# Kernel optimization log

Hardware: AMD Instinct MI355X
Metric: run time of the kernel (lower is better)

## Reference

```python
import jax, jax.numpy as jnp
import numpy as np

HIDDEN = 256
HEADS = 8
HEAD_DIM = HIDDEN // HEADS
BATCH = 2
N_NODES = 8192
N_EDGES = 262144


def setup_inputs() -> dict:
    key = jax.random.key(0)
    ks = jax.random.split(key, 12)
    node_states = jax.random.normal(ks[0], (BATCH, N_NODES, HIDDEN), dtype=jnp.float32)
    b_idx = jax.random.randint(ks[1], (N_EDGES,), 0, BATCH)
    s_idx = jax.random.randint(ks[2], (N_EDGES,), 0, N_NODES)
    t_idx = jax.random.randint(ks[3], (N_EDGES,), 0, N_NODES)
    edge_indices = jnp.stack([b_idx, s_idx, t_idx]).astype(jnp.int64)
    edge_values = jax.random.normal(ks[4], (N_EDGES, HIDDEN), dtype=jnp.float32)
    scale = 1.0 / np.sqrt(HIDDEN)
    Wq = jax.random.normal(ks[5], (HIDDEN, HIDDEN), dtype=jnp.float32) * scale
    bq = jnp.zeros((HIDDEN,), jnp.float32)
    Wk = jax.random.normal(ks[6], (HIDDEN, HIDDEN), dtype=jnp.float32) * scale
    bk = jnp.zeros((HIDDEN,), jnp.float32)
    Wv = jax.random.normal(ks[7], (HIDDEN, HIDDEN), dtype=jnp.float32) * scale
    bv = jnp.zeros((HIDDEN,), jnp.float32)
    We = jax.random.normal(ks[8], (HIDDEN, HIDDEN), dtype=jnp.float32) * scale
    be = jnp.zeros((HIDDEN,), jnp.float32)
    return {"node_states": node_states, "edge_indices": edge_indices, "edge_values": edge_values,
            "Wq": Wq, "bq": bq, "Wk": Wk, "bk": bk, "Wv": Wv, "bv": bv, "We": We, "be": be}


def reference(node_states, edge_indices, edge_values, Wq, bq, Wk, bk, Wv, bv, We, be):
    batch, n_nodes, hidden = node_states.shape
    E = edge_indices.shape[1]
    b_idx, s_idx, t_idx = edge_indices[0], edge_indices[1], edge_indices[2]

    # Dense QKV projections over nodes (torch Linear: x @ W.T + b)
    Q = node_states @ Wq.T + bq
    K = node_states @ Wk.T + bk
    V = node_states @ Wv.T + bv

    # Gather per-edge query/key/value, split heads -> (E, H, D)
    Qm = Q[b_idx, s_idx].reshape(E, HEADS, HEAD_DIM)
    Kn = K[b_idx, t_idx].reshape(E, HEADS, HEAD_DIM)
    Vn = V[b_idx, t_idx].reshape(E, HEADS, HEAD_DIM)

    # Edge feature projections (use_edge_values=True path)
    Ke = (edge_values @ Wk.T + bk).reshape(E, HEADS, HEAD_DIM)
    Ve = (edge_values @ We.T + be).reshape(E, HEADS, HEAD_DIM)

    inv_sqrt_d = 1.0 / jnp.sqrt(jnp.float32(HEAD_DIM))
    # node2node + node2edge = Qm.(Kn+Ke)/sqrt(d)  -> (E, H)
    logits = jnp.sum(Qm * (Kn + Ke), axis=-1) * inv_sqrt_d

    # torch.sparse.softmax(..., dim=-1): dim -1 of (B,N,N,H) is the DENSE heads
    # dim, so softmax is taken over the heads axis of the per-edge values.
    attn = jax.nn.softmax(logits, axis=-1)  # (E, H)

    out_edges = (attn[..., None] * (Vn + Ve)).reshape(E, hidden)  # (E, hidden)

    # Scatter-sum edges to their (batch, src) node: sparse.mm with 0/1 mask
    seg = b_idx * n_nodes + s_idx
    flat = jax.ops.segment_sum(out_edges, seg, num_segments=batch * n_nodes)
    return flat.reshape(batch, n_nodes, hidden)
```

## Files before the change

### kernel.cpp

```cpp
#include <hip/hip_runtime.h>
#include <hip/hip_bf16.h>

#define HID 256
#define NN 8192
#define NE 262144

typedef float f32x4 __attribute__((ext_vector_type(4)));
typedef __bf16 bf16x8 __attribute__((ext_vector_type(8)));
typedef __bf16 bf16x4 __attribute__((ext_vector_type(4)));

__global__ void conv_weights(const float* __restrict__ wq, const float* __restrict__ wk,
                             const float* __restrict__ wv, const float* __restrict__ we,
                             __bf16* __restrict__ o) {
    int i = blockIdx.x * 256 + threadIdx.x;
    const float* srcs[4] = {wq, wk, wv, we};
    int m = i >> 16;
    int j = i & 65535;
    o[i] = (__bf16)srcs[m][j];
}

__device__ __forceinline__ void stage_tile(const float* __restrict__ src, char* lb, int tid) {
    const float4* xs = (const float4*)src;
    #pragma unroll
    for (int kq = 0; kq < 16; ++kq) {
        int f = tid + kq * 256;
        int row = f >> 6, c4 = f & 63;
        float4 v = xs[f];
        bf16x4 h;
        h[0] = (__bf16)v.x; h[1] = (__bf16)v.y; h[2] = (__bf16)v.z; h[3] = (__bf16)v.w;
        int off = (row * 512 + c4 * 8) ^ ((row & 7) << 4);
        *(bf16x4*)(lb + off) = h;
    }
}

__global__ void qkv_gemm(const float* __restrict__ x,
                         const __bf16* __restrict__ wbf,
                         const float* __restrict__ bq, const float* __restrict__ bk,
                         const float* __restrict__ bv,
                         __bf16* __restrict__ qbf, __bf16* __restrict__ kbf,
                         __bf16* __restrict__ vbf) {
    __shared__ __bf16 xt[64 * 256];
    char* lb = (char*)xt;
    int tid = threadIdx.x;
    int blk = blockIdx.x;

    stage_tile(x + (size_t)blk * 64 * 256, lb, tid);
    __syncthreads();

    int w = tid >> 6, lane = tid & 63;
    int l15 = lane & 15, l4 = lane >> 4;
    int cw = w * 64;
    const float* biases[3] = {bq, bk, bv};
    __bf16* outs[3] = {qbf, kbf, vbf};

    for (int m = 0; m < 3; ++m) {
        const __bf16* W = wbf + (size_t)m * 65536;
        f32x4 acc[4][4] = {};
        for (int ks = 0; ks < 8; ++ks) {
            bf16x8 aW[4], bE[4];
            #pragma unroll
            for (int tn = 0; tn < 4; ++tn)
                aW[tn] = *(const bf16x8*)(W + (size_t)(cw + tn * 16 + l15) * 256 + ks * 32 + l4 * 8);
            #pragma unroll
            for (int te = 0; te < 4; ++te) {
                int row = te * 16 + l15;
                int off = (row * 512 + ks * 64 + l4 * 16) ^ ((row & 7) << 4);
                bE[te] = *(const bf16x8*)(lb + off);
            }
            #pragma unroll
            for (int tn = 0; tn < 4; ++tn)
                #pragma unroll
                for (int te = 0; te < 4; ++te)
                    acc[tn][te] = __builtin_amdgcn_mfma_f32_16x16x32_bf16(aW[tn], bE[te], acc[tn][te], 0, 0, 0);
        }
        __bf16* out = outs[m];
        #pragma unroll
        for (int tn = 0; tn < 4; ++tn) {
            float4 b4 = *(const float4*)(biases[m] + cw + tn * 16 + l4 * 4);
            #pragma unroll
            for (int te = 0; te < 4; ++te) {
                int row = blk * 64 + te * 16 + l15;
                int col = cw + tn * 16 + l4 * 4;
                bf16x4 h;
                h[0] = (__bf16)(acc[tn][te][0] + b4.x);
                h[1] = (__bf16)(acc[tn][te][1] + b4.y);
                h[2] = (__bf16)(acc[tn][te][2] + b4.z);
                h[3] = (__bf16)(acc[tn][te][3] + b4.w);
                *(bf16x4*)(out + (size_t)row * 256 + col) = h;
            }
        }
    }
}

__global__ void k_hist(const int* __restrict__ eidx, unsigned* __restrict__ hist) {
    int e = blockIdx.x * 256 + threadIdx.x;
    int key = eidx[e] * NN + eidx[NE + e];
    atomicAdd(&hist[key], 1u);
}

__global__ void k_scan(const unsigned* __restrict__ hist, unsigned* __restrict__ cursor) {
    __shared__ unsigned tot[256];
    int tid = threadIdx.x;
    unsigned s = 0;
    for (int i = 0; i < 64; ++i) s += hist[tid * 64 + i];
    tot[tid] = s;
    __syncthreads();
    for (int d = 1; d < 256; d <<= 1) {
        unsigned v = (tid >= d) ? tot[tid - d] : 0u;
        __syncthreads();
        tot[tid] += v;
        __syncthreads();
    }
    unsigned run = (tid == 0) ? 0u : tot[tid - 1];
    for (int i = 0; i < 64; ++i) {
        int idx = tid * 64 + i;
        cursor[idx] = run;
        run += hist[idx];
    }
}

__global__ void k_perm(const int* __restrict__ eidx, unsigned* __restrict__ cursor,
                       int* __restrict__ perm) {
    int e = blockIdx.x * 256 + threadIdx.x;
    int key = eidx[e] * NN + eidx[NE + e];
    unsigned pos = atomicAdd(&cursor[key], 1u);
    perm[pos] = e;
}

__global__ void edge_logits(const float* __restrict__ ev,
                            const int* __restrict__ eidx,
                            const __bf16* __restrict__ wbf,
                            const float* __restrict__ bkb,
                            const __bf16* __restrict__ qbf, const __bf16* __restrict__ kbf,
                            float* __restrict__ attn_ws) {
    __shared__ __bf16 evt[64 * 256];
    __shared__ int sb[64], ss[64], st[64];
    char* lb = (char*)evt;
    int tid = threadIdx.x;
    int e0 = blockIdx.x * 64;

    stage_tile(ev + (size_t)e0 * 256, lb, tid);
    if (tid < 64) {
        sb[tid] = eidx[e0 + tid];
        ss[tid] = eidx[NE + e0 + tid];
        st[tid] = eidx[2 * NE + e0 + tid];
    }
    __syncthreads();

    int w = tid >> 6, lane = tid & 63;
    int l15 = lane & 15, l4 = lane >> 4;
    int cw = w * 64;

    const __bf16* WK = wbf + 65536;
    f32x4 acc[4][4] = {};
    for (int ks = 0; ks < 8; ++ks) {
        bf16x8 aW[4], bE[4];
        #pragma unroll
        for (int tn = 0; tn < 4; ++tn)
            aW[tn] = *(const bf16x8*)(WK + (size_t)(cw + tn * 16 + l15) * 256 + ks * 32 + l4 * 8);
        #pragma unroll
        for (int te = 0; te < 4; ++te) {
            int row = te * 16 + l15;
            int off = (row * 512 + ks * 64 + l4 * 16) ^ ((row & 7) << 4);
            bE[te] = *(const bf16x8*)(lb + off);
        }
        #pragma unroll
        for (int tn = 0; tn < 4; ++tn)
            #pragma unroll
            for (int te = 0; te < 4; ++te)
                acc[tn][te] = __builtin_amdgcn_mfma_f32_16x16x32_bf16(aW[tn], bE[te], acc[tn][te], 0, 0, 0);
    }
    __syncthreads();

    #pragma unroll
    for (int tn = 0; tn < 4; ++tn) {
        float4 b4 = *(const float4*)(bkb + cw + tn * 16 + l4 * 4);
        #pragma unroll
        for (int te = 0; te < 4; ++te) {
            int edge = te * 16 + l15;
            int colb = (cw + tn * 16 + l4 * 4) * 2;
            bf16x4 h;
            h[0] = (__bf16)(acc[tn][te][0] + b4.x);
            h[1] = (__bf16)(acc[tn][te][1] + b4.y);
            h[2] = (__bf16)(acc[tn][te][2] + b4.z);
            h[3] = (__bf16)(acc[tn][te][3] + b4.w);
            int off = (edge * 512 + colb) ^ ((edge & 7) << 4);
            *(bf16x4*)(lb + off) = h;
        }
    }
    __syncthreads();

    int cl = lane & 31, eh = lane >> 5;
    #pragma unroll
    for (int it = 0; it < 8; ++it) {
        int e = w * 16 + it * 2 + eh;
        int b_ = sb[e], s_ = ss[e], t_ = st[e];
        bf16x8 qv = *(const bf16x8*)(qbf + ((size_t)b_ * NN + s_) * 256 + cl * 8);
        bf16x8 kv = *(const bf16x8*)(kbf + ((size_t)b_ * NN + t_) * 256 + cl * 8);
        int off = (e * 512 + cl * 16) ^ ((e & 7) << 4);
        bf16x8 kev = *(const bf16x8*)(lb + off);
        float val = 0.f;
        #pragma unroll
        for (int j = 0; j < 8; ++j)
            val += (float)qv[j] * ((float)kv[j] + (float)kev[j]);
        val += __shfl_xor(val, 1);
        val += __shfl_xor(val, 2);
        val *= 0.17677669529663687f;
        float mx = val;
        mx = fmaxf(mx, __shfl_xor(mx, 4));
        mx = fmaxf(mx, __shfl_xor(mx, 8));
        mx = fmaxf(mx, __shfl_xor(mx, 16));
        float ex = __expf(val - mx);
        float s4 = ex;
        s4 += __shfl_xor(s4, 4);
        s4 += __shfl_xor(s4, 8);
        s4 += __shfl_xor(s4, 16);
        float a = ex / s4;
        if ((cl & 3) == 0)
            attn_ws[(size_t)(e0 + e) * 8 + (cl >> 2)] = a;
    }
}

__global__ void edge_scatter2(const float* __restrict__ ev,
                              const int* __restrict__ eidx,
                              const __bf16* __restrict__ wbf,
                              const float* __restrict__ beb,
                              const __bf16* __restrict__ vbf,
                              const float* __restrict__ attn_ws,
                              const int* __restrict__ perm,
                              float* __restrict__ out) {
    __shared__ __bf16 evt[64 * 256];
    __shared__ int pe[64], sb[64], ss[64], st[64];
    char* lb = (char*)evt;
    int tid = threadIdx.x;
    int p0 = blockIdx.x * 64;

    if (tid < 64) {
        int e = perm[p0 + tid];
        pe[tid] = e;
        sb[tid] = eidx[e];
        ss[tid] = eidx[NE + e];
        st[tid] = eidx[2 * NE + e];
    }
    __syncthreads();

    #pragma unroll
    for (int kq = 0; kq < 16; ++kq) {
        int f = tid + kq * 256;
        int row = f >> 6, c4 = f & 63;
        const float4* src = (const float4*)(ev + (size_t)pe[row] * 256);
        float4 v = src[c4];
        bf16x4 h;
        h[0] = (__bf16)v.x; h[1] = (__bf16)v.y; h[2] = (__bf16)v.z; h[3] = (__bf16)v.w;
        int off = (row * 512 + c4 * 8) ^ ((row & 7) << 4);
        *(bf16x4*)(lb + off) = h;
    }
    __syncthreads();

    int w = tid >> 6, lane = tid & 63;
    int l15 = lane & 15, l4 = lane >> 4;
    int cw = w * 64;

    const __bf16* WE = wbf + 3 * 65536;
    f32x4 acc[4][4] = {};
    for (int ks = 0; ks < 8; ++ks) {
        bf16x8 aW[4], bE[4];
        #pragma unroll
        for (int tn = 0; tn < 4; ++tn)
            aW[tn] = *(const bf16x8*)(WE + (size_t)(cw + tn * 16 + l15) * 256 + ks * 32 + l4 * 8);
        #pragma unroll
        for (int te = 0; te < 4; ++te) {
            int row = te * 16 + l15;
            int off = (row * 512 + ks * 64 + l4 * 16) ^ ((row & 7) << 4);
            bE[te] = *(const bf16x8*)(lb + off);
        }
        #pragma unroll
        for (int tn = 0; tn < 4; ++tn)
            #pragma unroll
            for (int te = 0; te < 4; ++te)
                acc[tn][te] = __builtin_amdgcn_mfma_f32_16x16x32_bf16(aW[tn], bE[te], acc[tn][te], 0, 0, 0);
    }
    __syncthreads();

    #pragma unroll
    for (int tn = 0; tn < 4; ++tn) {
        float4 b4 = *(const float4*)(beb + cw + tn * 16 + l4 * 4);
        #pragma unroll
        for (int te = 0; te < 4; ++te) {
            int edge = te * 16 + l15;
            int colb = (cw + tn * 16 + l4 * 4) * 2;
            bf16x4 h;
            h[0] = (__bf16)(acc[tn][te][0] + b4.x);
            h[1] = (__bf16)(acc[tn][te][1] + b4.y);
            h[2] = (__bf16)(acc[tn][te][2] + b4.z);
            h[3] = (__bf16)(acc[tn][te][3] + b4.w);
            int off = (edge * 512 + colb) ^ ((edge & 7) << 4);
            *(bf16x4*)(lb + off) = h;
        }
    }
    __syncthreads();

    float a0 = 0.f, a1 = 0.f, a2 = 0.f, a3 = 0.f;
    int havekey = -1;
    size_t obase = 0;
    #pragma unroll
    for (int it = 0; it < 16; ++it) {
        int e = w * 16 + it;
        int ge = pe[e];
        int b_ = sb[e], s_ = ss[e], t_ = st[e];
        const __bf16* vrow = vbf + ((size_t)b_ * NN + t_) * 256;
        int swz = (e & 7) << 4;
        float c0, c1, c2, c3;
        {
            float att, vv, vev;
            int col, off;
            col = lane;             att = attn_ws[(size_t)ge * 8 + 0 + (lane >> 5)];
            vv = (float)vrow[col];  off = (e * 512 + col * 2) ^ swz;
            vev = (float)*(const __bf16*)(lb + off); c0 = att * (vv + vev);
            col = 64 + lane;        att = attn_ws[(size_t)ge * 8 + 2 + (lane >> 5)];
            vv = (float)vrow[col];  off = (e * 512 + col * 2) ^ swz;
            vev = (float)*(const __bf16*)(lb + off); c1 = att * (vv + vev);
            col = 128 + lane;       att = attn_ws[(size_t)ge * 8 + 4 + (lane >> 5)];
            vv = (float)vrow[col];  off = (e * 512 + col * 2) ^ swz;
            vev = (float)*(const __bf16*)(lb + off); c2 = att * (vv + vev);
            col = 192 + lane;       att = attn_ws[(size_t)ge * 8 + 6 + (lane >> 5)];
            vv = (float)vrow[col];  off = (e * 512 + col * 2) ^ swz;
            vev = (float)*(const __bf16*)(lb + off); c3 = att * (vv + vev);
        }
        int key = __builtin_amdgcn_readfirstlane(b_ * NN + s_);
        if (key != havekey) {
            if (havekey >= 0) {
                float* orow = out + obase;
                unsafeAtomicAdd(orow + lane, a0);
                unsafeAtomicAdd(orow + 64 + lane, a1);
                unsafeAtomicAdd(orow + 128 + lane, a2);
                unsafeAtomicAdd(orow + 192 + lane, a3);
            }
            a0 = c0; a1 = c1; a2 = c2; a3 = c3;
            havekey = key;
            obase = (size_t)key * 256;
        } else {
            a0 += c0; a1 += c1; a2 += c2; a3 += c3;
        }
    }
    if (havekey >= 0) {
        float* orow = out + obase;
        unsafeAtomicAdd(orow + lane, a0);
        unsafeAtomicAdd(orow + 64 + lane, a1);
        unsafeAtomicAdd(orow + 128 + lane, a2);
        unsafeAtomicAdd(orow + 192 + lane, a3);
    }
}

extern "C" void kernel_launch(void* const* d_in, const int* in_sizes, int n_in,
                              void* d_out, int out_size, void* d_ws, size_t ws_size,
                              hipStream_t stream) {
    const float* node_states = (const float*)d_in[0];
    const int*   eidx        = (const int*)d_in[1];
    const float* ev          = (const float*)d_in[2];
    const float* Wq          = (const float*)d_in[3];
    const float* bq          = (const float*)d_in[4];
    const float* Wk          = (const float*)d_in[5];
    const float* bk          = (const float*)d_in[6];
    const float* Wv          = (const float*)d_in[7];
    const float* bv          = (const float*)d_in[8];
    const float* We          = (const float*)d_in[9];
    const float* be          = (const float*)d_in[10];
    float* out = (float*)d_out;

    char* ws = (char*)d_ws;
    __bf16*   qbf     = (__bf16*)ws;
    __bf16*   kbf     = (__bf16*)(ws + 8388608);
    __bf16*   vbf     = (__bf16*)(ws + 16777216);
    float*    attn_ws = (float*)(ws + 25165824);
    __bf16*   wbf     = (__bf16*)(ws + 33554432);
    unsigned* hist    = (unsigned*)(ws + 34078720);
    unsigned* cursor  = (unsigned*)(ws + 34144256);
    int*      perm    = (int*)(ws + 34209792);

    hipMemsetAsync(d_out, 0, (size_t)out_size * sizeof(float), stream);
    hipMemsetAsync(hist, 0, 16384 * sizeof(unsigned), stream);
    conv_weights<<<1024, 256, 0, stream>>>(Wq, Wk, Wv, We, wbf);
    qkv_gemm<<<256, 256, 0, stream>>>(node_states, wbf, bq, bk, bv, qbf, kbf, vbf);
    k_hist<<<1024, 256, 0, stream>>>(eidx, hist);
    k_scan<<<1, 256, 0, stream>>>(hist, cursor);
    k_perm<<<1024, 256, 0, stream>>>(eidx, cursor, perm);
    edge_logits<<<4096, 256, 0, stream>>>(ev, eidx, wbf, bk, qbf, kbf, attn_ws);
    edge_scatter2<<<4096, 256, 0, stream>>>(ev, eidx, wbf, be, vbf, attn_ws, perm, out);
}
```

Baseline: 332.9 us.

## Fuse edge logits and scatter kernels, keep attention weights in LDS

Merges the logits and scatter kernels into one kernel that stages each permuted edge tile once, computes the Ke projection and logits straight from MFMA accumulators, and runs the per-edge softmax in shared memory. This removes the second full read and conversion of edge_values and the global attention workspace round-trip. In exchange the kernel holds more live state, which risks register pressure under the occupancy-4 launch bound, and the logits stage now gathers Q/K rows in permuted order.

```diff
diff --git a/kernel.cpp b/kernel.cpp
--- a/kernel.cpp
+++ b/kernel.cpp
@@ -127,110 +127,18 @@
     perm[pos] = e;
 }
 
-__global__ void edge_logits(const float* __restrict__ ev,
-                            const int* __restrict__ eidx,
-                            const __bf16* __restrict__ wbf,
-                            const float* __restrict__ bkb,
-                            const __bf16* __restrict__ qbf, const __bf16* __restrict__ kbf,
-                            float* __restrict__ attn_ws) {
-    __shared__ __bf16 evt[64 * 256];
-    __shared__ int sb[64], ss[64], st[64];
-    char* lb = (char*)evt;
-    int tid = threadIdx.x;
-    int e0 = blockIdx.x * 64;
-
-    stage_tile(ev + (size_t)e0 * 256, lb, tid);
-    if (tid < 64) {
-        sb[tid] = eidx[e0 + tid];
-        ss[tid] = eidx[NE + e0 + tid];
-        st[tid] = eidx[2 * NE + e0 + tid];
-    }
-    __syncthreads();
-
-    int w = tid >> 6, lane = tid & 63;
-    int l15 = lane & 15, l4 = lane >> 4;
-    int cw = w * 64;
-
-    const __bf16* WK = wbf + 65536;
-    f32x4 acc[4][4] = {};
-    for (int ks = 0; ks < 8; ++ks) {
-        bf16x8 aW[4], bE[4];
-        #pragma unroll
-        for (int tn = 0; tn < 4; ++tn)
-            aW[tn] = *(const bf16x8*)(WK + (size_t)(cw + tn * 16 + l15) * 256 + ks * 32 + l4 * 8);
-        #pragma unroll
-        for (int te = 0; te < 4; ++te) {
-            int row = te * 16 + l15;
-            int off = (row * 512 + ks * 64 + l4 * 16) ^ ((row & 7) << 4);
-            bE[te] = *(const bf16x8*)(lb + off);
-        }
-        #pragma unroll
-        for (int tn = 0; tn < 4; ++tn)
-            #pragma unroll
-            for (int te = 0; te < 4; ++te)
-                acc[tn][te] = __builtin_amdgcn_mfma_f32_16x16x32_bf16(aW[tn], bE[te], acc[tn][te], 0, 0, 0);
-    }
-    __syncthreads();
-
-    #pragma unroll
-    for (int tn = 0; tn < 4; ++tn) {
-        float4 b4 = *(const float4*)(bkb + cw + tn * 16 + l4 * 4);
-        #pragma unroll
-        for (int te = 0; te < 4; ++te) {
-            int edge = te * 16 + l15;
-            int colb = (cw + tn * 16 + l4 * 4) * 2;
-            bf16x4 h;
-            h[0] = (__bf16)(acc[tn][te][0] + b4.x);
-            h[1] = (__bf16)(acc[tn][te][1] + b4.y);
-            h[2] = (__bf16)(acc[tn][te][2] + b4.z);
-            h[3] = (__bf16)(acc[tn][te][3] + b4.w);
-            int off = (edge * 512 + colb) ^ ((edge & 7) << 4);
-            *(bf16x4*)(lb + off) = h;
-        }
-    }
-    __syncthreads();
-
-    int cl = lane & 31, eh = lane >> 5;
-    #pragma unroll
-    for (int it = 0; it < 8; ++it) {
-        int e = w * 16 + it * 2 + eh;
-        int b_ = sb[e], s_ = ss[e], t_ = st[e];
-        bf16x8 qv = *(const bf16x8*)(qbf + ((size_t)b_ * NN + s_) * 256 + cl * 8);
-        bf16x8 kv = *(const bf16x8*)(kbf + ((size_t)b_ * NN + t_) * 256 + cl * 8);
-        int off = (e * 512 + cl * 16) ^ ((e & 7) << 4);
-        bf16x8 kev = *(const bf16x8*)(lb + off);
-        float val = 0.f;
-        #pragma unroll
-        for (int j = 0; j < 8; ++j)
-            val += (float)qv[j] * ((float)kv[j] + (float)kev[j]);
-        val += __shfl_xor(val, 1);
-        val += __shfl_xor(val, 2);
-        val *= 0.17677669529663687f;
-        float mx = val;
-        mx = fmaxf(mx, __shfl_xor(mx, 4));
-        mx = fmaxf(mx, __shfl_xor(mx, 8));
-        mx = fmaxf(mx, __shfl_xor(mx, 16));
-        float ex = __expf(val - mx);
-        float s4 = ex;
-        s4 += __shfl_xor(s4, 4);
-        s4 += __shfl_xor(s4, 8);
-        s4 += __shfl_xor(s4, 16);
-        float a = ex / s4;
-        if ((cl & 3) == 0)
-            attn_ws[(size_t)(e0 + e) * 8 + (cl >> 2)] = a;
-    }
-}
-
-__global__ void edge_scatter2(const float* __restrict__ ev,
-                              const int* __restrict__ eidx,
-                              const __bf16* __restrict__ wbf,
-                              const float* __restrict__ beb,
-                              const __bf16* __restrict__ vbf,
-                              const float* __restrict__ attn_ws,
-                              const int* __restrict__ perm,
-                              float* __restrict__ out) {
+__global__ __launch_bounds__(256, 4)
+void edge_fused(const float* __restrict__ ev,
+                const int* __restrict__ eidx,
+                const __bf16* __restrict__ wbf,
+                const float* __restrict__ bkb, const float* __restrict__ beb,
+                const __bf16* __restrict__ qbf, const __bf16* __restrict__ kbf,
+                const __bf16* __restrict__ vbf,
+                const int* __restrict__ perm,
+                float* __restrict__ out) {
     __shared__ __bf16 evt[64 * 256];
     __shared__ int pe[64], sb[64], ss[64], st[64];
+    __shared__ float smx[64 * 8];
     char* lb = (char*)evt;
     int tid = threadIdx.x;
     int p0 = blockIdx.x * 64;
@@ -261,41 +169,113 @@
     int l15 = lane & 15, l4 = lane >> 4;
     int cw = w * 64;
 
-    const __bf16* WE = wbf + 3 * 65536;
-    f32x4 acc[4][4] = {};
-    for (int ks = 0; ks < 8; ++ks) {
-        bf16x8 aW[4], bE[4];
+    {
+        const __bf16* WK = wbf + 65536;
+        f32x4 acc[4][4] = {};
+        for (int ks = 0; ks < 8; ++ks) {
+            bf16x8 aW[4], bE[4];
+            #pragma unroll
+            for (int tn = 0; tn < 4; ++tn)
+                aW[tn] = *(const bf16x8*)(WK + (size_t)(cw + tn * 16 + l15) * 256 + ks * 32 + l4 * 8);
+            #pragma unroll
+            for (int te = 0; te < 4; ++te) {
+                int row = te * 16 + l15;
+                int off = (row * 512 + ks * 64 + l4 * 16) ^ ((row & 7) << 4);
+                bE[te] = *(const bf16x8*)(lb + off);
+            }
+            #pragma unroll
+            for (int tn = 0; tn < 4; ++tn)
+                #pragma unroll
+                for (int te = 0; te < 4; ++te)
+                    acc[tn][te] = __builtin_amdgcn_mfma_f32_16x16x32_bf16(aW[tn], bE[te], acc[tn][te], 0, 0, 0);
+        }
+
+        f32x4 bk4[4];
         #pragma unroll
         for (int tn = 0; tn < 4; ++tn)
-            aW[tn] = *(const bf16x8*)(WE + (size_t)(cw + tn * 16 + l15) * 256 + ks * 32 + l4 * 8);
+            bk4[tn] = *(const f32x4*)(bkb + cw + tn * 16 + l4 * 4);
+
         #pragma unroll
         for (int te = 0; te < 4; ++te) {
-            int row = te * 16 + l15;
-            int off = (row * 512 + ks * 64 + l4 * 16) ^ ((row & 7) << 4);
-            bE[te] = *(const bf16x8*)(lb + off);
-        }
-        #pragma unroll
-        for (int tn = 0; tn < 4; ++tn)
-            #pragma unroll
-            for (int te = 0; te < 4; ++te)
-                acc[tn][te] = __builtin_amdgcn_mfma_f32_16x16x32_bf16(aW[tn], bE[te], acc[tn][te], 0, 0, 0);
-    }
-    __syncthreads();
-
-    #pragma unroll
-    for (int tn = 0; tn < 4; ++tn) {
-        float4 b4 = *(const float4*)(beb + cw + tn * 16 + l4 * 4);
-        #pragma unroll
-        for (int te = 0; te < 4; ++te) {
-            int edge = te * 16 + l15;
-            int colb = (cw + tn * 16 + l4 * 4) * 2;
-            bf16x4 h;
-            h[0] = (__bf16)(acc[tn][te][0] + b4.x);
-            h[1] = (__bf16)(acc[tn][te][1] + b4.y);
-            h[2] = (__bf16)(acc[tn][te][2] + b4.z);
-            h[3] = (__bf16)(acc[tn][te][3] + b4.w);
-            int off = (edge * 512 + colb) ^ ((edge & 7) << 4);
-            *(bf16x4*)(lb + off) = h;
+            int el = te * 16 + l15;
+            int b_ = sb[el], s_ = ss[el], t_ = st[el];
+            const __bf16* qp = qbf + ((size_t)b_ * NN + s_) * 256 + cw + l4 * 4;
+            const __bf16* kp = kbf + ((size_t)b_ * NN + t_) * 256 + cw + l4 * 4;
+            bf16x4 qv[4], kv[4];
+            #pragma unroll
+            for (int tn = 0; tn < 4; ++tn) {
+                qv[tn] = *(const bf16x4*)(qp + tn * 16);
+                kv[tn] = *(const bf16x4*)(kp + tn * 16);
+            }
+            #pragma unroll
+            for (int h = 0; h < 2; ++h) {
+                float val = 0.f;
+                #pragma unroll
+                for (int j = 0; j < 2; ++j) {
+                    int tn = h * 2 + j;
+                    #pragma unroll
+                    for (int r = 0; r < 4; ++r) {
+                        float ke = acc[tn][te][r] + bk4[tn][r];
+                        val += (float)qv[tn][r] * ((float)kv[tn][r] + ke);
+                    }
+                }
+                val += __shfl_xor(val, 16);
+                val += __shfl_xor(val, 32);
+                if (l4 == 0) smx[el * 8 + w * 2 + h] = val * 0.17677669529663687f;
+            }
+        }
+    }
+    __syncthreads();
+
+    if (tid < 64) {
+        float l[8], mx = -1e30f;
+        #pragma unroll
+        for (int h = 0; h < 8; ++h) { l[h] = smx[tid * 8 + h]; mx = fmaxf(mx, l[h]); }
+        float sum = 0.f;
+        #pragma unroll
+        for (int h = 0; h < 8; ++h) { l[h] = __expf(l[h] - mx); sum += l[h]; }
+        float inv = 1.f / sum;
+        #pragma unroll
+        for (int h = 0; h < 8; ++h) smx[tid * 8 + h] = l[h] * inv;
+    }
+
+    {
+        const __bf16* WE = wbf + 3 * 65536;
+        f32x4 acc[4][4] = {};
+        for (int ks = 0; ks < 8; ++ks) {
+            bf16x8 aW[4], bE[4];
+            #pragma unroll
+            for (int tn = 0; tn < 4; ++tn)
+                aW[tn] = *(const bf16x8*)(WE + (size_t)(cw + tn * 16 + l15) * 256 + ks * 32 + l4 * 8);
+            #pragma unroll
+            for (int te = 0; te < 4; ++te) {
+                int row = te * 16 + l15;
+                int off = (row * 512 + ks * 64 + l4 * 16) ^ ((row & 7) << 4);
+                bE[te] = *(const bf16x8*)(lb + off);
+            }
+            #pragma unroll
+            for (int tn = 0; tn < 4; ++tn)
+                #pragma unroll
+                for (int te = 0; te < 4; ++te)
+                    acc[tn][te] = __builtin_amdgcn_mfma_f32_16x16x32_bf16(aW[tn], bE[te], acc[tn][te], 0, 0, 0);
+        }
+        __syncthreads();
+
+        #pragma unroll
+        for (int tn = 0; tn < 4; ++tn) {
+            float4 b4 = *(const float4*)(beb + cw + tn * 16 + l4 * 4);
+            #pragma unroll
+            for (int te = 0; te < 4; ++te) {
+                int edge = te * 16 + l15;
+                int colb = (cw + tn * 16 + l4 * 4) * 2;
+                bf16x4 h;
+                h[0] = (__bf16)(acc[tn][te][0] + b4.x);
+                h[1] = (__bf16)(acc[tn][te][1] + b4.y);
+                h[2] = (__bf16)(acc[tn][te][2] + b4.z);
+                h[3] = (__bf16)(acc[tn][te][3] + b4.w);
+                int off = (edge * 512 + colb) ^ ((edge & 7) << 4);
+                *(bf16x4*)(lb + off) = h;
+            }
         }
     }
     __syncthreads();
@@ -306,7 +286,6 @@
     #pragma unroll
     for (int it = 0; it < 16; ++it) {
         int e = w * 16 + it;
-        int ge = pe[e];
         int b_ = sb[e], s_ = ss[e], t_ = st[e];
         const __bf16* vrow = vbf + ((size_t)b_ * NN + t_) * 256;
         int swz = (e & 7) << 4;
@@ -314,16 +293,16 @@
         {
             float att, vv, vev;
             int col, off;
-            col = lane;             att = attn_ws[(size_t)ge * 8 + 0 + (lane >> 5)];
+            col = lane;             att = smx[e * 8 + 0 + (lane >> 5)];
             vv = (float)vrow[col];  off = (e * 512 + col * 2) ^ swz;
             vev = (float)*(const __bf16*)(lb + off); c0 = att * (vv + vev);
-            col = 64 + lane;        att = attn_ws[(size_t)ge * 8 + 2 + (lane >> 5)];
+            col = 64 + lane;        att = smx[e * 8 + 2 + (lane >> 5)];
             vv = (float)vrow[col];  off = (e * 512 + col * 2) ^ swz;
             vev = (float)*(const __bf16*)(lb + off); c1 = att * (vv + vev);
-            col = 128 + lane;       att = attn_ws[(size_t)ge * 8 + 4 + (lane >> 5)];
+            col = 128 + lane;       att = smx[e * 8 + 4 + (lane >> 5)];
             vv = (float)vrow[col];  off = (e * 512 + col * 2) ^ swz;
             vev = (float)*(const __bf16*)(lb + off); c2 = att * (vv + vev);
-            col = 192 + lane;       att = attn_ws[(size_t)ge * 8 + 6 + (lane >> 5)];
+            col = 192 + lane;       att = smx[e * 8 + 6 + (lane >> 5)];
             vv = (float)vrow[col];  off = (e * 512 + col * 2) ^ swz;
             vev = (float)*(const __bf16*)(lb + off); c3 = att * (vv + vev);
         }
@@ -369,14 +348,13 @@
     float* out = (float*)d_out;
 
     char* ws = (char*)d_ws;
-    __bf16*   qbf     = (__bf16*)ws;
-    __bf16*   kbf     = (__bf16*)(ws + 8388608);
-    __bf16*   vbf     = (__bf16*)(ws + 16777216);
-    float*    attn_ws = (float*)(ws + 25165824);
-    __bf16*   wbf     = (__bf16*)(ws + 33554432);
-    unsigned* hist    = (unsigned*)(ws + 34078720);
-    unsigned* cursor  = (unsigned*)(ws + 34144256);
-    int*      perm    = (int*)(ws + 34209792);
+    __bf16*   qbf    = (__bf16*)ws;
+    __bf16*   kbf    = (__bf16*)(ws + 8388608);
+    __bf16*   vbf    = (__bf16*)(ws + 16777216);
+    __bf16*   wbf    = (__bf16*)(ws + 25165824);
+    unsigned* hist   = (unsigned*)(ws + 25690112);
+    unsigned* cursor = (unsigned*)(ws + 25755648);
+    int*      perm   = (int*)(ws + 25821184);
 
     hipMemsetAsync(d_out, 0, (size_t)out_size * sizeof(float), stream);
     hipMemsetAsync(hist, 0, 16384 * sizeof(unsigned), stream);
@@ -385,6 +363,5 @@
     k_hist<<<1024, 256, 0, stream>>>(eidx, hist);
     k_scan<<<1, 256, 0, stream>>>(hist, cursor);
     k_perm<<<1024, 256, 0, stream>>>(eidx, cursor, perm);
-    edge_logits<<<4096, 256, 0, stream>>>(ev, eidx, wbf, bk, qbf, kbf, attn_ws);
-    edge_scatter2<<<4096, 256, 0, stream>>>(ev, eidx, wbf, be, vbf, attn_ws, perm, out);
-}
+    edge_fused<<<4096, 256, 0, stream>>>(ev, eidx, wbf, bk, be, qbf, kbf, vbf, perm, out);
+}
```

Result: slower. 358.2 us (+7.6%).

## Fuse edge logits and scatter kernels into one permuted-edge kernel

Applied to the files above, without the earlier changes.

Merges the edge-logit/softmax kernel and the edge scatter kernel into a single kernel over permuted edges. The edge-value tile is staged once and both the Wk and We projections are computed from it in one MFMA loop. Attention weights stay in shared memory instead of going through a global workspace. Q/K gathers are hoisted ahead of the GEMM so they can overlap it. In exchange, doubling the accumulators (ak and av) raises register pressure under a launch bound of 4 waves, which risks spills or lower occupancy.

```diff
diff --git a/kernel.cpp b/kernel.cpp
--- a/kernel.cpp
+++ b/kernel.cpp
@@ -127,37 +127,69 @@
     perm[pos] = e;
 }
 
-__global__ void edge_logits(const float* __restrict__ ev,
-                            const int* __restrict__ eidx,
-                            const __bf16* __restrict__ wbf,
-                            const float* __restrict__ bkb,
-                            const __bf16* __restrict__ qbf, const __bf16* __restrict__ kbf,
-                            float* __restrict__ attn_ws) {
+__global__ __launch_bounds__(256, 4)
+void edge_fused2(const float* __restrict__ ev,
+                 const int* __restrict__ eidx,
+                 const __bf16* __restrict__ wbf,
+                 const float* __restrict__ bkb, const float* __restrict__ beb,
+                 const __bf16* __restrict__ qbf, const __bf16* __restrict__ kbf,
+                 const __bf16* __restrict__ vbf,
+                 const int* __restrict__ perm,
+                 float* __restrict__ out) {
     __shared__ __bf16 evt[64 * 256];
-    __shared__ int sb[64], ss[64], st[64];
+    __shared__ int pe[64], sb[64], ss[64], st[64];
+    __shared__ float smx[64 * 8];
     char* lb = (char*)evt;
     int tid = threadIdx.x;
-    int e0 = blockIdx.x * 64;
-
-    stage_tile(ev + (size_t)e0 * 256, lb, tid);
+    int p0 = blockIdx.x * 64;
+
     if (tid < 64) {
-        sb[tid] = eidx[e0 + tid];
-        ss[tid] = eidx[NE + e0 + tid];
-        st[tid] = eidx[2 * NE + e0 + tid];
+        int e = perm[p0 + tid];
+        pe[tid] = e;
+        sb[tid] = eidx[e];
+        ss[tid] = eidx[NE + e];
+        st[tid] = eidx[2 * NE + e];
+    }
+    __syncthreads();
+
+    #pragma unroll
+    for (int kq = 0; kq < 16; ++kq) {
+        int f = tid + kq * 256;
+        int row = f >> 6, c4 = f & 63;
+        const float4* src = (const float4*)(ev + (size_t)pe[row] * 256);
+        float4 v = src[c4];
+        bf16x4 h;
+        h[0] = (__bf16)v.x; h[1] = (__bf16)v.y; h[2] = (__bf16)v.z; h[3] = (__bf16)v.w;
+        int off = (row * 512 + c4 * 8) ^ ((row & 7) << 4);
+        *(bf16x4*)(lb + off) = h;
     }
     __syncthreads();
 
     int w = tid >> 6, lane = tid & 63;
     int l15 = lane & 15, l4 = lane >> 4;
     int cw = w * 64;
+    int cl = lane & 31, eh = lane >> 5;
+
+    bf16x8 qv[8], kv[8];
+    #pragma unroll
+    for (int it = 0; it < 8; ++it) {
+        int e = w * 16 + it * 2 + eh;
+        int b_ = sb[e], s_ = ss[e], t_ = st[e];
+        qv[it] = *(const bf16x8*)(qbf + ((size_t)b_ * NN + s_) * 256 + cl * 8);
+        kv[it] = *(const bf16x8*)(kbf + ((size_t)b_ * NN + t_) * 256 + cl * 8);
+    }
 
     const __bf16* WK = wbf + 65536;
-    f32x4 acc[4][4] = {};
+    const __bf16* WE = wbf + 3 * 65536;
+    f32x4 ak[4][4] = {}, av[4][4] = {};
     for (int ks = 0; ks < 8; ++ks) {
-        bf16x8 aW[4], bE[4];
-        #pragma unroll
-        for (int tn = 0; tn < 4; ++tn)
-            aW[tn] = *(const bf16x8*)(WK + (size_t)(cw + tn * 16 + l15) * 256 + ks * 32 + l4 * 8);
+        bf16x8 aK[4], aE[4], bE[4];
+        #pragma unroll
+        for (int tn = 0; tn < 4; ++tn) {
+            size_t wo = (size_t)(cw + tn * 16 + l15) * 256 + ks * 32 + l4 * 8;
+            aK[tn] = *(const bf16x8*)(WK + wo);
+            aE[tn] = *(const bf16x8*)(WE + wo);
+        }
         #pragma unroll
         for (int te = 0; te < 4; ++te) {
             int row = te * 16 + l15;
@@ -167,8 +199,10 @@
         #pragma unroll
         for (int tn = 0; tn < 4; ++tn)
             #pragma unroll
-            for (int te = 0; te < 4; ++te)
-                acc[tn][te] = __builtin_amdgcn_mfma_f32_16x16x32_bf16(aW[tn], bE[te], acc[tn][te], 0, 0, 0);
+            for (int te = 0; te < 4; ++te) {
+                ak[tn][te] = __builtin_amdgcn_mfma_f32_16x16x32_bf16(aK[tn], bE[te], ak[tn][te], 0, 0, 0);
+                av[tn][te] = __builtin_amdgcn_mfma_f32_16x16x32_bf16(aE[tn], bE[te], av[tn][te], 0, 0, 0);
+            }
     }
     __syncthreads();
 
@@ -180,29 +214,25 @@
             int edge = te * 16 + l15;
             int colb = (cw + tn * 16 + l4 * 4) * 2;
             bf16x4 h;
-            h[0] = (__bf16)(acc[tn][te][0] + b4.x);
-            h[1] = (__bf16)(acc[tn][te][1] + b4.y);
-            h[2] = (__bf16)(acc[tn][te][2] + b4.z);
-            h[3] = (__bf16)(acc[tn][te][3] + b4.w);
+            h[0] = (__bf16)(ak[tn][te][0] + b4.x);
+            h[1] = (__bf16)(ak[tn][te][1] + b4.y);
+            h[2] = (__bf16)(ak[tn][te][2] + b4.z);
+            h[3] = (__bf16)(ak[tn][te][3] + b4.w);
             int off = (edge * 512 + colb) ^ ((edge & 7) << 4);
             *(bf16x4*)(lb + off) = h;
         }
     }
     __syncthreads();
 
-    int cl = lane & 31, eh = lane >> 5;
     #pragma unroll
     for (int it = 0; it < 8; ++it) {
         int e = w * 16 + it * 2 + eh;
-        int b_ = sb[e], s_ = ss[e], t_ = st[e];
-        bf16x8 qv = *(const bf16x8*)(qbf + ((size_t)b_ * NN + s_) * 256 + cl * 8);
-        bf16x8 kv = *(const bf16x8*)(kbf + ((size_t)b_ * NN + t_) * 256 + cl * 8);
         int off = (e * 512 + cl * 16) ^ ((e & 7) << 4);
         bf16x8 kev = *(const bf16x8*)(lb + off);
         float val = 0.f;
         #pragma unroll
         for (int j = 0; j < 8; ++j)
-            val += (float)qv[j] * ((float)kv[j] + (float)kev[j]);
+            val += (float)qv[it][j] * ((float)kv[it][j] + (float)kev[j]);
         val += __shfl_xor(val, 1);
         val += __shfl_xor(val, 2);
         val *= 0.17677669529663687f;
@@ -217,68 +247,7 @@
         s4 += __shfl_xor(s4, 16);
         float a = ex / s4;
         if ((cl & 3) == 0)
-            attn_ws[(size_t)(e0 + e) * 8 + (cl >> 2)] = a;
-    }
-}
-
-__global__ void edge_scatter2(const float* __restrict__ ev,
-                              const int* __restrict__ eidx,
-                              const __bf16* __restrict__ wbf,
-                              const float* __restrict__ beb,
-                              const __bf16* __restrict__ vbf,
-                              const float* __restrict__ attn_ws,
-                              const int* __restrict__ perm,
-                              float* __restrict__ out) {
-    __shared__ __bf16 evt[64 * 256];
-    __shared__ int pe[64], sb[64], ss[64], st[64];
-    char* lb = (char*)evt;
-    int tid = threadIdx.x;
-    int p0 = blockIdx.x * 64;
-
-    if (tid < 64) {
-        int e = perm[p0 + tid];
-        pe[tid] = e;
-        sb[tid] = eidx[e];
-        ss[tid] = eidx[NE + e];
-        st[tid] = eidx[2 * NE + e];
-    }
-    __syncthreads();
-
-    #pragma unroll
-    for (int kq = 0; kq < 16; ++kq) {
-        int f = tid + kq * 256;
-        int row = f >> 6, c4 = f & 63;
-        const float4* src = (const float4*)(ev + (size_t)pe[row] * 256);
-        float4 v = src[c4];
-        bf16x4 h;
-        h[0] = (__bf16)v.x; h[1] = (__bf16)v.y; h[2] = (__bf16)v.z; h[3] = (__bf16)v.w;
-        int off = (row * 512 + c4 * 8) ^ ((row & 7) << 4);
-        *(bf16x4*)(lb + off) = h;
-    }
-    __syncthreads();
-
-    int w = tid >> 6, lane = tid & 63;
-    int l15 = lane & 15, l4 = lane >> 4;
-    int cw = w * 64;
-
-    const __bf16* WE = wbf + 3 * 65536;
-    f32x4 acc[4][4] = {};
-    for (int ks = 0; ks < 8; ++ks) {
-        bf16x8 aW[4], bE[4];
-        #pragma unroll
-        for (int tn = 0; tn < 4; ++tn)
-            aW[tn] = *(const bf16x8*)(WE + (size_t)(cw + tn * 16 + l15) * 256 + ks * 32 + l4 * 8);
-        #pragma unroll
-        for (int te = 0; te < 4; ++te) {
-            int row = te * 16 + l15;
-            int off = (row * 512 + ks * 64 + l4 * 16) ^ ((row & 7) << 4);
-            bE[te] = *(const bf16x8*)(lb + off);
-        }
-        #pragma unroll
-        for (int tn = 0; tn < 4; ++tn)
-            #pragma unroll
-            for (int te = 0; te < 4; ++te)
-                acc[tn][te] = __builtin_amdgcn_mfma_f32_16x16x32_bf16(aW[tn], bE[te], acc[tn][te], 0, 0, 0);
+            smx[e * 8 + (cl >> 2)] = a;
     }
     __syncthreads();
 
@@ -290,10 +259,10 @@
             int edge = te * 16 + l15;
             int colb = (cw + tn * 16 + l4 * 4) * 2;
             bf16x4 h;
-            h[0] = (__bf16)(acc[tn][te][0] + b4.x);
-            h[1] = (__bf16)(acc[tn][te][1] + b4.y);
-            h[2] = (__bf16)(acc[tn][te][2] + b4.z);
-            h[3] = (__bf16)(acc[tn][te][3] + b4.w);
+            h[0] = (__bf16)(av[tn][te][0] + b4.x);
+            h[1] = (__bf16)(av[tn][te][1] + b4.y);
+            h[2] = (__bf16)(av[tn][te][2] + b4.z);
+            h[3] = (__bf16)(av[tn][te][3] + b4.w);
             int off = (edge * 512 + colb) ^ ((edge & 7) << 4);
             *(bf16x4*)(lb + off) = h;
         }
@@ -306,7 +275,6 @@
     #pragma unroll
     for (int it = 0; it < 16; ++it) {
         int e = w * 16 + it;
-        int ge = pe[e];
         int b_ = sb[e], s_ = ss[e], t_ = st[e];
         const __bf16* vrow = vbf + ((size_t)b_ * NN + t_) * 256;
         int swz = (e & 7) << 4;
@@ -314,16 +282,16 @@
         {
             float att, vv, vev;
             int col, off;
-            col = lane;             att = attn_ws[(size_t)ge * 8 + 0 + (lane >> 5)];
+            col = lane;             att = smx[e * 8 + 0 + (lane >> 5)];
             vv = (float)vrow[col];  off = (e * 512 + col * 2) ^ swz;
             vev = (float)*(const __bf16*)(lb + off); c0 = att * (vv + vev);
-            col = 64 + lane;        att = attn_ws[(size_t)ge * 8 + 2 + (lane >> 5)];
+            col = 64 + lane;        att = smx[e * 8 + 2 + (lane >> 5)];
             vv = (float)vrow[col];  off = (e * 512 + col * 2) ^ swz;
             vev = (float)*(const __bf16*)(lb + off); c1 = att * (vv + vev);
-            col = 128 + lane;       att = attn_ws[(size_t)ge * 8 + 4 + (lane >> 5)];
+            col = 128 + lane;       att = smx[e * 8 + 4 + (lane >> 5)];
             vv = (float)vrow[col];  off = (e * 512 + col * 2) ^ swz;
             vev = (float)*(const __bf16*)(lb + off); c2 = att * (vv + vev);
-            col = 192 + lane;       att = attn_ws[(size_t)ge * 8 + 6 + (lane >> 5)];
+            col = 192 + lane;       att = smx[e * 8 + 6 + (lane >> 5)];
             vv = (float)vrow[col];  off = (e * 512 + col * 2) ^ swz;
             vev = (float)*(const __bf16*)(lb + off); c3 = att * (vv + vev);
         }
@@ -369,14 +337,13 @@
     float* out = (float*)d_out;
 
     char* ws = (char*)d_ws;
-    __bf16*   qbf     = (__bf16*)ws;
-    __bf16*   kbf     = (__bf16*)(ws + 8388608);
-    __bf16*   vbf     = (__bf16*)(ws + 16777216);
-    float*    attn_ws = (float*)(ws + 25165824);
-    __bf16*   wbf     = (__bf16*)(ws + 33554432);
-    unsigned* hist    = (unsigned*)(ws + 34078720);
-    unsigned* cursor  = (unsigned*)(ws + 34144256);
-    int*      perm    = (int*)(ws + 34209792);
+    __bf16*   qbf    = (__bf16*)ws;
+    __bf16*   kbf    = (__bf16*)(ws + 8388608);
+    __bf16*   vbf    = (__bf16*)(ws + 16777216);
+    __bf16*   wbf    = (__bf16*)(ws + 25165824);
+    unsigned* hist   = (unsigned*)(ws + 25690112);
+    unsigned* cursor = (unsigned*)(ws + 25755648);
+    int*      perm   = (int*)(ws + 25821184);
 
     hipMemsetAsync(d_out, 0, (size_t)out_size * sizeof(float), stream);
     hipMemsetAsync(hist, 0, 16384 * sizeof(unsigned), stream);
@@ -385,6 +352,5 @@
     k_hist<<<1024, 256, 0, stream>>>(eidx, hist);
     k_scan<<<1, 256, 0, stream>>>(hist, cursor);
     k_perm<<<1024, 256, 0, stream>>>(eidx, cursor, perm);
-    edge_logits<<<4096, 256, 0, stream>>>(ev, eidx, wbf, bk, qbf, kbf, attn_ws);
-    edge_scatter2<<<4096, 256, 0, stream>>>(ev, eidx, wbf, be, vbf, attn_ws, perm, out);
-}
+    edge_fused2<<<4096, 256, 0, stream>>>(ev, eidx, wbf, bk, be, qbf, kbf, vbf, perm, out);
+}
```

New measurement: 734.8 us. +120.7%, slower.
